# Optimization experiments

Hardware: AMD Instinct MI355X
Metric: run time of the kernel (lower is better)

The kernel has to match this reference:

```python
import jax, jax.numpy as jnp
import numpy as np


def setup_inputs() -> dict:
    key = jax.random.key(0)
    k1, k2, k3 = jax.random.split(key, 3)
    B, T, I, H = 128, 1024, 256, 512
    scale = 1.0 / np.sqrt(I + H)
    return {
        "x": jax.random.normal(k1, (B, T, I), dtype=jnp.float32),
        "Wz": jax.random.normal(k2, (I + H, H), dtype=jnp.float32) * scale,
        "bz": jnp.zeros((H,), dtype=jnp.float32),
        "Wh": jax.random.normal(k3, (I + H, H), dtype=jnp.float32) * scale,
        "bh": jnp.zeros((H,), dtype=jnp.float32),
    }


def reference(x, Wz, bz, Wh, bh):
    # x: (B, T, I); returns (outputs (B, T, H), h_last (B, H))
    B, T, I = x.shape
    H = Wz.shape[1]
    # split weights into input/hidden parts to avoid per-step concat
    Wz_x, Wz_h = Wz[:I], Wz[I:]
    Wh_x, Wh_h = Wh[:I], Wh[I:]
    # precompute input projections for all timesteps (one big GEMM each)
    xz = jnp.einsum("bti,ih->bth", x, Wz_x) + bz  # (B, T, H)
    xh = jnp.einsum("bti,ih->bth", x, Wh_x) + bh  # (B, T, H)

    def step(h_prev, inp):
        xz_t, xh_t = inp
        z_t = jax.nn.sigmoid(xz_t + h_prev @ Wz_h)
        h_tilde = jnp.tanh(xh_t + h_prev @ Wh_h)
        h_t = (1.0 - z_t) * h_prev + z_t * h_tilde
        return h_t, h_t

    h0 = jnp.zeros((B, H), dtype=x.dtype)
    # scan over time: inputs shaped (T, B, H)
    h_last, outs = jax.lax.scan(
        step, h0, (jnp.swapaxes(xz, 0, 1), jnp.swapaxes(xh, 0, 1))
    )
    outputs = jnp.swapaxes(outs, 0, 1)  # (B, T, H)
    return outputs, h_last
```

## Files before the change

kernel.cpp:

```cpp
#include <hip/hip_runtime.h>
#include <stdint.h>


#define Bb 128
#define Tt 1024
#define Ii 256
#define Hh 512
#define HB_PAR (8 * 16 * 256)
#define FLAGS_OFF (2 * HB_PAR)
#define NFLAG_W 256

typedef short short8 __attribute__((ext_vector_type(8)));
typedef float float4_ __attribute__((ext_vector_type(4)));
typedef unsigned int uint4_ __attribute__((ext_vector_type(4)));

__device__ __forceinline__ unsigned short f2bf(float f) {
  union { float f; uint32_t u; } v; v.f = f;
  uint32_t r = v.u + 0x7FFFu + ((v.u >> 16) & 1u);
  return (unsigned short)(r >> 16);
}

__global__ void prep_kernel(uint32_t* ws) {
  int i = blockIdx.x * 256 + threadIdx.x;
  if (i < NFLAG_W) ws[FLAGS_OFF + i] = 0u;
}

__global__ __launch_bounds__(512, 2) void mingru_kernel(
    const float* __restrict__ x, const float* __restrict__ Wz,
    const float* __restrict__ bz, const float* __restrict__ Wh,
    const float* __restrict__ bh, float* __restrict__ out,
    uint32_t* __restrict__ hbuf) {
  const int bg = blockIdx.x & 7;
  const int cs = blockIdx.x >> 3;
  const int tid = threadIdx.x;
  const int wave = tid >> 6;
  const int lane = tid & 63;
  const int lm = lane & 15;
  const int quad = lane >> 4;
  const int is_h = (wave >> 2) & 1;
  const int tile = wave & 3;
  const int wcol = cs * 64 + tile * 16 + lm;
  const float* W = is_h ? Wh : Wz;

  uint32_t* ctrp = hbuf + FLAGS_OFF + (size_t)bg * 32;

  short8 wx[8], wh[16];
#pragma unroll
  for (int s = 0; s < 8; ++s) {
    union { unsigned short e[8]; short8 v; } u;
#pragma unroll
    for (int j = 0; j < 8; ++j)
      u.e[j] = f2bf(W[(size_t)(s * 32 + quad * 8 + j) * Hh + wcol]);
    wx[s] = u.v;
  }
#pragma unroll
  for (int s = 0; s < 16; ++s) {
    union { unsigned short e[8]; short8 v; } u;
#pragma unroll
    for (int j = 0; j < 8; ++j)
      u.e[j] = f2bf(W[(size_t)(Ii + s * 32 + quad * 8 + j) * Hh + wcol]);
    wh[s] = u.v;
  }

  __shared__ uint32_t hs[16 * 260];
  __shared__ float S[2][16][66];

  const int em = tid >> 5;
  const int ec = (tid & 31) << 1;
  const int ecolg = cs * 64 + ec;
  const int eb = bg * 16 + em;
  const float bz0 = bz[ecolg], bz1 = bz[ecolg + 1];
  const float bh0 = bh[ecolg], bh1 = bh[ecolg + 1];
  float hp0 = 0.f, hp1 = 0.f;
  float* outp = out + (size_t)eb * (Tt * Hh) + ecolg;
  const uint32_t epair = (uint32_t)((bg * 16 + em) * 256 + (ecolg >> 1));

  const float* xlane = x + (size_t)(bg * 16 + lm) * (Tt * Ii) + quad * 8;
  float4_ xf[16];
#pragma unroll
  for (int s = 0; s < 8; ++s) {
    xf[2 * s] = *(const float4_*)(xlane + 32 * s);
    xf[2 * s + 1] = *(const float4_*)(xlane + 32 * s + 4);
  }

  for (int t = 0; t < Tt; ++t) {
    float4_ acc = {0.f, 0.f, 0.f, 0.f};
    float4_ acc2 = {0.f, 0.f, 0.f, 0.f};
#pragma unroll
    for (int s = 0; s < 8; ++s) {
      float4_ a0 = xf[2 * s];
      float4_ a1 = xf[2 * s + 1];
      union { unsigned short e[8]; short8 v; } u;
      u.e[0] = f2bf(a0[0]); u.e[1] = f2bf(a0[1]);
      u.e[2] = f2bf(a0[2]); u.e[3] = f2bf(a0[3]);
      u.e[4] = f2bf(a1[0]); u.e[5] = f2bf(a1[1]);
      u.e[6] = f2bf(a1[2]); u.e[7] = f2bf(a1[3]);
      if (s & 1)
        acc2 = __builtin_amdgcn_mfma_f32_16x16x32_bf16(u.v, wx[s], acc2, 0, 0, 0);
      else
        acc = __builtin_amdgcn_mfma_f32_16x16x32_bf16(u.v, wx[s], acc, 0, 0, 0);
    }

    if (t > 0) {
      if (tid == 0) {
        const uint32_t tgt = 8u * (uint32_t)t;
        int spins = 0;
        while (__hip_atomic_load(ctrp, __ATOMIC_RELAXED,
                                 __HIP_MEMORY_SCOPE_AGENT) < tgt) {
          if (++spins > (1 << 18)) break;
        }
      }
      __syncthreads();
      {
        unsigned long long* hq =
            (unsigned long long*)(hbuf + ((t - 1) & 1) * HB_PAR) + (size_t)bg * 2048;
#pragma unroll
        for (int k = 0; k < 4; ++k) {
          int g = tid + 512 * k;
          unsigned long long v = __hip_atomic_load(hq + g, __ATOMIC_RELAXED,
                                                   __HIP_MEMORY_SCOPE_AGENT);
          int m = g >> 7, c = g & 127;
          *(unsigned long long*)&hs[m * 260 + c * 2] = v;
        }
      }
      __syncthreads();
    }

    {
      const float* xp = xlane + (size_t)((t + 1 < Tt) ? t + 1 : t) * Ii;
#pragma unroll
      for (int s = 0; s < 8; ++s) {
        xf[2 * s] = *(const float4_*)(xp + 32 * s);
        xf[2 * s + 1] = *(const float4_*)(xp + 32 * s + 4);
      }
    }

    if (t > 0) {
#pragma unroll
      for (int s = 0; s < 16; ++s) {
        uint4_ d = *(const uint4_*)&hs[lm * 260 + s * 16 + quad * 4];
        union { uint4_ q; short8 v; } u; u.q = d;
        if (s & 1)
          acc2 = __builtin_amdgcn_mfma_f32_16x16x32_bf16(u.v, wh[s], acc2, 0, 0, 0);
        else
          acc = __builtin_amdgcn_mfma_f32_16x16x32_bf16(u.v, wh[s], acc, 0, 0, 0);
      }
    }

    S[is_h][quad * 4 + 0][tile * 16 + lm] = acc[0] + acc2[0];
    S[is_h][quad * 4 + 1][tile * 16 + lm] = acc[1] + acc2[1];
    S[is_h][quad * 4 + 2][tile * 16 + lm] = acc[2] + acc2[2];
    S[is_h][quad * 4 + 3][tile * 16 + lm] = acc[3] + acc2[3];
    __syncthreads();

    float sz0 = S[0][em][ec]     + bz0;
    float sz1 = S[0][em][ec + 1] + bz1;
    float sh0 = S[1][em][ec]     + bh0;
    float sh1 = S[1][em][ec + 1] + bh1;
    float z0 = 1.f / (1.f + __expf(-sz0));
    float z1 = 1.f / (1.f + __expf(-sz1));
    float g0 = 1.f - 2.f / (1.f + __expf(2.f * sh0));
    float g1 = 1.f - 2.f / (1.f + __expf(2.f * sh1));
    hp0 += z0 * (g0 - hp0);
    hp1 += z1 * (g1 - hp1);

    uint32_t pk = (uint32_t)f2bf(hp0) | ((uint32_t)f2bf(hp1) << 16);
    __hip_atomic_store(hbuf + (t & 1) * HB_PAR + epair, pk,
                       __ATOMIC_RELAXED, __HIP_MEMORY_SCOPE_AGENT);
    __builtin_amdgcn_s_waitcnt(0);
    __syncthreads();
    if (tid == 0)
      __hip_atomic_fetch_add(ctrp, 1u, __ATOMIC_RELAXED, __HIP_MEMORY_SCOPE_AGENT);

    float2 ov; ov.x = hp0; ov.y = hp1;
    *(float2*)(outp + (size_t)t * Hh) = ov;
    if (t == Tt - 1)
      *(float2*)(out + (size_t)Bb * Tt * Hh + (size_t)eb * Hh + ecolg) = ov;
  }
}

extern "C" void kernel_launch(void* const* d_in, const int* in_sizes, int n_in,
                              void* d_out, int out_size, void* d_ws, size_t ws_size,
                              hipStream_t stream) {
  const float* x  = (const float*)d_in[0];
  const float* Wz = (const float*)d_in[1];
  const float* bz = (const float*)d_in[2];
  const float* Wh = (const float*)d_in[3];
  const float* bh = (const float*)d_in[4];
  float* out = (float*)d_out;
  uint32_t* hbuf = (uint32_t*)d_ws;

  prep_kernel<<<dim3(1), dim3(256), 0, stream>>>(hbuf);
  mingru_kernel<<<dim3(64), dim3(512), 0, stream>>>(x, Wz, bz, Wh, bh, out, hbuf);
}
```

Before: 6.158 ms.

## Replace counter barrier with poison-sentinel data polling over four-slot hidden buffer

Removes the per-step atomic counter, the waitcnt, and one syncthreads. Each thread now polls its own 32 bytes of the previous step's hidden state until no word equals a poison sentinel, and re-poisons the slot two steps ahead. This turns the serial flag handshake into data-carried readiness across a 4-slot ring, which shortens the critical path of each recurrence step. The costs are extra memory traffic from uncached polling loads, reliance on store ordering and atomicity at word granularity, and a larger prep kernel that initialises all slots.

```diff
diff --git a/kernel.cpp b/kernel.cpp
--- a/kernel.cpp
+++ b/kernel.cpp
@@ -7,8 +7,8 @@
 #define Ii 256
 #define Hh 512
 #define HB_PAR (8 * 16 * 256)
-#define FLAGS_OFF (2 * HB_PAR)
-#define NFLAG_W 256
+#define NSLOT 4
+#define POISON 0xFFFFFFFFu
 
 typedef short short8 __attribute__((ext_vector_type(8)));
 typedef float float4_ __attribute__((ext_vector_type(4)));
@@ -22,7 +22,17 @@
 
 __global__ void prep_kernel(uint32_t* ws) {
   int i = blockIdx.x * 256 + threadIdx.x;
-  if (i < NFLAG_W) ws[FLAGS_OFF + i] = 0u;
+  if (i < NSLOT * HB_PAR) ws[i] = POISON;
+}
+
+__device__ __forceinline__ void poll32(const uint32_t* p, uint4_& a, uint4_& b) {
+  asm volatile(
+      "global_load_dwordx4 %0, %2, off sc0 sc1\n\t"
+      "global_load_dwordx4 %1, %2, off offset:16 sc0 sc1\n\t"
+      "s_waitcnt vmcnt(0)"
+      : "=&v"(a), "=&v"(b)
+      : "v"(p)
+      : "memory");
 }
 
 __global__ __launch_bounds__(512, 2) void mingru_kernel(
@@ -41,8 +51,6 @@
   const int tile = wave & 3;
   const int wcol = cs * 64 + tile * 16 + lm;
   const float* W = is_h ? Wh : Wz;
-
-  uint32_t* ctrp = hbuf + FLAGS_OFF + (size_t)bg * 32;
 
   short8 wx[8], wh[16];
 #pragma unroll
@@ -102,28 +110,27 @@
     }
 
     if (t > 0) {
-      if (tid == 0) {
-        const uint32_t tgt = 8u * (uint32_t)t;
-        int spins = 0;
-        while (__hip_atomic_load(ctrp, __ATOMIC_RELAXED,
-                                 __HIP_MEMORY_SCOPE_AGENT) < tgt) {
-          if (++spins > (1 << 18)) break;
+      {
+        const uint32_t* pp =
+            hbuf + (size_t)((t - 1) & 3) * HB_PAR + bg * 4096 + 8 * tid;
+        uint4_ d0, d1;
+        int rounds = 0;
+        for (;;) {
+          poll32(pp, d0, d1);
+          int ok = (d0[0] != POISON) & (d0[1] != POISON) &
+                   (d0[2] != POISON) & (d0[3] != POISON) &
+                   (d1[0] != POISON) & (d1[1] != POISON) &
+                   (d1[2] != POISON) & (d1[3] != POISON);
+          if (ok || ++rounds > (1 << 12)) break;
         }
+        const int m = tid >> 5;
+        const int c0 = 8 * (tid & 31);
+        *(uint4_*)&hs[m * 260 + c0] = d0;
+        *(uint4_*)&hs[m * 260 + c0 + 4] = d1;
       }
       __syncthreads();
-      {
-        unsigned long long* hq =
-            (unsigned long long*)(hbuf + ((t - 1) & 1) * HB_PAR) + (size_t)bg * 2048;
-#pragma unroll
-        for (int k = 0; k < 4; ++k) {
-          int g = tid + 512 * k;
-          unsigned long long v = __hip_atomic_load(hq + g, __ATOMIC_RELAXED,
-                                                   __HIP_MEMORY_SCOPE_AGENT);
-          int m = g >> 7, c = g & 127;
-          *(unsigned long long*)&hs[m * 260 + c * 2] = v;
-        }
-      }
-      __syncthreads();
+      __hip_atomic_store(hbuf + (size_t)((t + 2) & 3) * HB_PAR + epair, POISON,
+                         __ATOMIC_RELAXED, __HIP_MEMORY_SCOPE_AGENT);
     }
 
     {
@@ -165,12 +172,8 @@
     hp1 += z1 * (g1 - hp1);
 
     uint32_t pk = (uint32_t)f2bf(hp0) | ((uint32_t)f2bf(hp1) << 16);
-    __hip_atomic_store(hbuf + (t & 1) * HB_PAR + epair, pk,
+    __hip_atomic_store(hbuf + (size_t)(t & 3) * HB_PAR + epair, pk,
                        __ATOMIC_RELAXED, __HIP_MEMORY_SCOPE_AGENT);
-    __builtin_amdgcn_s_waitcnt(0);
-    __syncthreads();
-    if (tid == 0)
-      __hip_atomic_fetch_add(ctrp, 1u, __ATOMIC_RELAXED, __HIP_MEMORY_SCOPE_AGENT);
 
     float2 ov; ov.x = hp0; ov.y = hp1;
     *(float2*)(outp + (size_t)t * Hh) = ov;
@@ -190,6 +193,6 @@
   float* out = (float*)d_out;
   uint32_t* hbuf = (uint32_t*)d_ws;
 
-  prep_kernel<<<dim3(1), dim3(256), 0, stream>>>(hbuf);
+  prep_kernel<<<dim3((NSLOT * HB_PAR + 255) / 256), dim3(256), 0, stream>>>(hbuf);
   mingru_kernel<<<dim3(64), dim3(512), 0, stream>>>(x, Wz, bz, Wh, bh, out, hbuf);
 }
```

After: 5.020 ms. 18.5% less time.
